# Kernel optimization log

Hardware: AMD Instinct MI355X
Metric: run time of the kernel (lower is better)

## Reference

```python
import jax, jax.numpy as jnp
import numpy as np


def setup_inputs() -> dict:
    key = jax.random.key(0)
    ks = jax.random.split(key, 6)
    B, C, H, W = 8, 128, 64, 64
    return {
        "curr_features": jax.random.normal(ks[0], (B, C, H, W), jnp.float32),
        "w1": jax.random.normal(ks[1], (C, 2 * C), jnp.float32) * 0.05,   # conv1x1 (2C->C)
        "b1": jnp.zeros((C,), jnp.float32),
        "gamma": jnp.ones((C,), jnp.float32),
        "beta": jnp.zeros((C,), jnp.float32),
        "running_mean": jax.random.normal(ks[2], (C,), jnp.float32) * 0.1,
        "running_var": jax.random.uniform(ks[3], (C,), jnp.float32, 0.5, 1.5),
        "w2": jax.random.normal(ks[4], (1, C), jnp.float32) * 0.05,       # conv1x1 (C->1)
        "b2": jnp.zeros((1,), jnp.float32),
    }


def reference(curr_features, w1, b1, gamma, beta, running_mean, running_var, w2, b2):
    B, C, H, W = curr_features.shape
    M = H * W
    BN_EPS = 1e-5
    LEAKY_SLOPE = 0.01  # InPlaceABNSync default activation: leaky_relu(0.01)

    f = curr_features.reshape(B, C, M)                       # [B,C,M]
    scores = jnp.einsum('bcm,bcn->bmn', f, f) * (C ** -0.5)  # [B,M,M]
    p = jax.nn.softmax(scores, axis=-1)
    feats1 = jnp.einsum('bmn,bcn->bcm', p, f)                # [B,C,M]

    x = jnp.concatenate([feats1, f], axis=1).reshape(B, 2 * C, H, W)

    # cls head: conv1x1 -> BN(inference) -> leaky_relu -> (dropout=identity in eval) -> conv1x1
    y = jnp.einsum('oc,bchw->bohw', w1, x) + b1[None, :, None, None]
    scale = gamma / jnp.sqrt(running_var + BN_EPS)
    y = (y - running_mean[None, :, None, None]) * scale[None, :, None, None] + beta[None, :, None, None]
    y = jnp.where(y >= 0, y, LEAKY_SLOPE * y)
    pred = jnp.einsum('oc,bchw->bohw', w2, y) + b2[None, :, None, None]  # [B,1,H,W]
    return pred
```

## Files before the change

kernel.cpp:

```cpp
#include <hip/hip_runtime.h>

#define NB 8
#define NC 128
#define NM 4096
#define FRAG 512

typedef __attribute__((ext_vector_type(8))) short short8;
typedef __attribute__((ext_vector_type(4))) float floatx4;

#define MFMA(a, b, c) __builtin_amdgcn_mfma_f32_16x16x32_bf16(a, b, c, 0, 0, 0)
#define EXP2F(x) __builtin_amdgcn_exp2f(x)

union S8U { short8 v; uint2 u2[2]; };

__device__ __forceinline__ unsigned pack2bf(float a, float b) {
    unsigned ua = __float_as_uint(a);
    unsigned ub = __float_as_uint(b);
    ua += 0x7fffu + ((ua >> 16) & 1u);
    ub += 0x7fffu + ((ub >> 16) & 1u);
    return (ua >> 16) | (ub & 0xffff0000u);
}

__device__ __forceinline__ unsigned cvt_pk_bf16(float a, float b) {
    unsigned r;
    asm("v_cvt_pk_bf16_f32 %0, %1, %2" : "=v"(r) : "v"(a), "v"(b));
    return r;
}

__constant__ float SF_C = 0.35712442f;
__constant__ float RS_C = 2.8001530f;


__global__ __launch_bounds__(256) void k_prep_f(
    const float* __restrict__ f, unsigned short* __restrict__ fX)
{
    __shared__ float Ls[128][65];
    const int tid = threadIdx.x;
    const int b   = blockIdx.x & 7;
    const int m0  = (blockIdx.x >> 3) * 64;
    const float* fb = f + (size_t)b * NC * NM;
    #pragma unroll
    for (int k = 0; k < 32; ++k) {
        int idx = tid + k * 256;
        int c = idx >> 6, mm = idx & 63;
        Ls[c][mm] = fb[(size_t)c * NM + m0 + mm];
    }
    __syncthreads();
    const float sf = SF_C;
    const int m  = tid >> 2;
    const int ks = tid & 3;
    const int ch = ks * 32;
    unsigned pk[16];
    #pragma unroll
    for (int i = 0; i < 16; ++i)
        pk[i] = pack2bf(Ls[ch + 2 * i][m] * sf, Ls[ch + 2 * i + 1][m] * sf);
    const int Mg  = m0 + m;
    const int mt  = Mg >> 4;
    const int lmm = Mg & 15;
    unsigned short* dst = fX + ((size_t)b * 256 + mt) * 4 * FRAG + ks * FRAG;
    #pragma unroll
    for (int q = 0; q < 4; ++q)
        *(uint4*)(dst + (q * 16 + lmm) * 8) =
            make_uint4(pk[4 * q], pk[4 * q + 1], pk[4 * q + 2], pk[4 * q + 3]);
}

__global__ __launch_bounds__(256) void k_prep_g(
    const unsigned short* __restrict__ fX, const float* __restrict__ w1,
    unsigned short* __restrict__ gX)
{
    __shared__ unsigned short gt[128][136];
    const int tid = threadIdx.x;
    const int wv  = tid >> 6;
    const int l   = tid & 63;
    const int lm  = l & 15;
    const int lq  = l >> 4;
    const int b    = blockIdx.x & 7;
    const int nblk = blockIdx.x >> 3;

    const float rs = RS_C;

    short8 wf2[2][4];
    #pragma unroll
    for (int j = 0; j < 2; ++j) {
        const int o = (wv * 2 + j) * 16 + lm;
        #pragma unroll
        for (int ks = 0; ks < 4; ++ks) {
            const float* wp = w1 + (size_t)o * (2 * NC) + ks * 32 + lq * 8;
            S8U t;
            t.u2[0] = make_uint2(pack2bf(wp[0] * rs, wp[1] * rs),
                                 pack2bf(wp[2] * rs, wp[3] * rs));
            t.u2[1] = make_uint2(pack2bf(wp[4] * rs, wp[5] * rs),
                                 pack2bf(wp[6] * rs, wp[7] * rs));
            wf2[j][ks] = t.v;
        }
    }

    const unsigned short* fXb = fX + (size_t)b * NM * NC;
    #pragma unroll 2
    for (int nt = 0; nt < 8; ++nt) {
        short8 af[4];
        #pragma unroll
        for (int ks = 0; ks < 4; ++ks)
            af[ks] = *(const short8*)
                (fXb + (size_t)(nblk * 8 + nt) * 4 * FRAG + ks * FRAG + l * 8);
        #pragma unroll
        for (int j = 0; j < 2; ++j) {
            floatx4 D = {0.f, 0.f, 0.f, 0.f};
            #pragma unroll
            for (int ks = 0; ks < 4; ++ks)
                D = MFMA(af[ks], wf2[j][ks], D);
            *(uint2*)&gt[(wv * 2 + j) * 16 + lm][nt * 16 + lq * 4] =
                make_uint2(pack2bf(D[0], D[1]), pack2bf(D[2], D[3]));
        }
    }
    __syncthreads();

    #pragma unroll
    for (int j = 0; j < 2; ++j) {
        const int ot = wv * 2 + j;
        #pragma unroll
        for (int k2 = 0; k2 < 4; ++k2) {
            uint4 v = *(const uint4*)&gt[ot * 16 + lm][k2 * 32 + lq * 8];
            *(uint4*)(gX + (((size_t)b * 32 + nblk) * 8 + ot) * 4 * FRAG
                      + k2 * FRAG + l * 8) = v;
        }
    }
}

__global__ __launch_bounds__(256, 2) void k_attn(
    const unsigned short* __restrict__ fX,
    const unsigned short* __restrict__ gX,
    const float* __restrict__ w1,
    const float* __restrict__ b1v, const float* __restrict__ gammav,
    const float* __restrict__ betav, const float* __restrict__ rmeanv,
    const float* __restrict__ rvarv, const float* __restrict__ w2v,
    const float* __restrict__ b2v, float* __restrict__ out)
{
    __shared__ __align__(16) char Ps[2][16384];
    __shared__ float lpart[4][64];
    __shared__ float opart[4][64];

    const int tid = threadIdx.x;
    const int w   = tid >> 6;
    const int l   = tid & 63;
    const int lm  = l & 15;
    const int lq  = l >> 4;
    const int b   = blockIdx.x & 7;
    const int m0  = (blockIdx.x >> 3) * 64;

    const int lq0 = lq & 1;
    const int lq1 = lq >> 1;
    const int lm3 = lm >> 3;
    const unsigned Xsw = (unsigned)(((lq1 << 1) | lm3) << 4);
    const unsigned wofsA =
        ((((unsigned)(w >> 1) * 4 * 16) + ((unsigned)(2 * (w & 1) + lq1) * 16)
          + (unsigned)lm) * 16 + (unsigned)(8 * lq0)) ^ Xsw;
    const unsigned rofs = ((unsigned)l * 16) ^ ((((unsigned)l >> 3) & 3u) << 4);

    const unsigned short* fXb = fX + (size_t)b * NM * NC;
    const unsigned short* gXb = gX + (size_t)b * NC * NM;

    short8 qf[4][4];
    {
        const int qt0 = m0 >> 4;
        #pragma unroll
        for (int mt = 0; mt < 4; ++mt)
            #pragma unroll
            for (int ks = 0; ks < 4; ++ks)
                qf[mt][ks] = *(const short8*)
                    (fXb + (size_t)(qt0 + mt) * 4 * FRAG + ks * FRAG + l * 8);
    }

    const unsigned short* kpA = fXb + (size_t)w * 4 * FRAG + l * 8;
    const unsigned short* kpB = fXb + (size_t)(4 + w) * 4 * FRAG + l * 8;
    const unsigned short* gp0 = gXb + (size_t)(2 * w) * 4 * FRAG + l * 8;
    const unsigned short* gp1 = gXb + (size_t)(2 * w + 1) * 4 * FRAG + l * 8;

    short8 kfA[4], kfB[4], gf0[4], gf1[4];
    #pragma unroll
    for (int ks = 0; ks < 4; ++ks) {
        kfA[ks] = *(const short8*)(kpA + ks * FRAG);
        kfB[ks] = *(const short8*)(kpB + ks * FRAG);
    }
    #pragma unroll
    for (int k2 = 0; k2 < 4; ++k2) {
        gf0[k2] = *(const short8*)(gp0 + k2 * FRAG);
        gf1[k2] = *(const short8*)(gp1 + k2 * FRAG);
    }

    floatx4 u[4][2];
    float lsum[4] = {0.f, 0.f, 0.f, 0.f};
    #pragma unroll
    for (int mt = 0; mt < 4; ++mt) {
        u[mt][0] = (floatx4){0.f, 0.f, 0.f, 0.f};
        u[mt][1] = (floatx4){0.f, 0.f, 0.f, 0.f};
    }

    floatx4 svA[4], svB[4];
    #pragma unroll
    for (int mt = 0; mt < 4; ++mt) {
        floatx4 a = {-24.f, -24.f, -24.f, -24.f};
        floatx4 bb = {-24.f, -24.f, -24.f, -24.f};
        #pragma unroll
        for (int ks = 0; ks < 4; ++ks) {
            a  = MFMA(kfA[ks], qf[mt][ks], a);
            bb = MFMA(kfB[ks], qf[mt][ks], bb);
        }
        svA[mt] = a; svB[mt] = bb;
    }
    kpA += 8 * 4 * FRAG; kpB += 8 * 4 * FRAG;
    #pragma unroll
    for (int ks = 0; ks < 4; ++ks) {
        kfA[ks] = *(const short8*)(kpA + ks * FRAG);
        kfB[ks] = *(const short8*)(kpB + ks * FRAG);
    }

    for (int it = 0; it < 32; ++it) {
        const int buf = it & 1;
        char* psb = Ps[buf];

        #pragma unroll
        for (int mt = 0; mt < 4; ++mt) {
            float pA0 = EXP2F(svA[mt][0]);
            float pA1 = EXP2F(svA[mt][1]);
            float pA2 = EXP2F(svA[mt][2]);
            float pA3 = EXP2F(svA[mt][3]);
            float pB0 = EXP2F(svB[mt][0]);
            float pB1 = EXP2F(svB[mt][1]);
            float pB2 = EXP2F(svB[mt][2]);
            float pB3 = EXP2F(svB[mt][3]);
            lsum[mt] += ((pA0 + pA1) + (pA2 + pA3)) +
                        ((pB0 + pB1) + (pB2 + pB3));
            *(uint2*)(psb + mt * 4096 + wofsA) =
                make_uint2(cvt_pk_bf16(pA0, pA1), cvt_pk_bf16(pA2, pA3));
            *(uint2*)(psb + mt * 4096 + wofsA + 2048) =
                make_uint2(cvt_pk_bf16(pB0, pB1), cvt_pk_bf16(pB2, pB3));

            floatx4 a = {-24.f, -24.f, -24.f, -24.f};
            floatx4 bb = {-24.f, -24.f, -24.f, -24.f};
            __builtin_amdgcn_s_setprio(1);
            #pragma unroll
            for (int ks = 0; ks < 4; ++ks) {
                a  = MFMA(kfA[ks], qf[mt][ks], a);
                bb = MFMA(kfB[ks], qf[mt][ks], bb);
            }
            __builtin_amdgcn_s_setprio(0);
            svA[mt] = a; svB[mt] = bb;
        }
        __syncthreads();

        {
            const int kstep = (it < 30) ? 8 * 4 * FRAG : 0;
            kpA += kstep; kpB += kstep;
            #pragma unroll
            for (int ks = 0; ks < 4; ++ks) {
                kfA[ks] = *(const short8*)(kpA + ks * FRAG);
                kfB[ks] = *(const short8*)(kpB + ks * FRAG);
            }
        }

        #pragma unroll
        for (int k2 = 0; k2 < 4; ++k2) {
            short8 pf[4];
            #pragma unroll
            for (int mt = 0; mt < 4; ++mt)
                pf[mt] = *(const short8*)(psb + mt * 4096 + k2 * 1024 + rofs);
            __builtin_amdgcn_s_setprio(1);
            #pragma unroll
            for (int mt = 0; mt < 4; ++mt) {
                u[mt][0] = MFMA(pf[mt], gf0[k2], u[mt][0]);
                u[mt][1] = MFMA(pf[mt], gf1[k2], u[mt][1]);
            }
            __builtin_amdgcn_s_setprio(0);
        }
        {
            const int gstep = (it < 31) ? 8 * 4 * FRAG : 0;
            gp0 += gstep; gp1 += gstep;
            #pragma unroll
            for (int k2 = 0; k2 < 4; ++k2) {
                gf0[k2] = *(const short8*)(gp0 + k2 * FRAG);
                gf1[k2] = *(const short8*)(gp1 + k2 * FRAG);
            }
        }
    }

    #pragma unroll
    for (int mt = 0; mt < 4; ++mt) {
        lsum[mt] += __shfl_xor(lsum[mt], 16);
        lsum[mt] += __shfl_xor(lsum[mt], 32);
    }
    if (lq == 0) {
        #pragma unroll
        for (int mt = 0; mt < 4; ++mt)
            lpart[w][mt * 16 + lm] = lsum[mt];
    }

    floatx4 hacc[4][2];
    {
        const float rs = RS_C;
        #pragma unroll
        for (int j = 0; j < 2; ++j) {
            int o = w * 32 + j * 16 + lm;
            short8 wf[4];
            #pragma unroll
            for (int ks = 0; ks < 4; ++ks) {
                const float* wp = w1 + (size_t)o * (2 * NC) + NC + ks * 32 + lq * 8;
                S8U t;
                t.u2[0] = make_uint2(pack2bf(wp[0] * rs, wp[1] * rs),
                                     pack2bf(wp[2] * rs, wp[3] * rs));
                t.u2[1] = make_uint2(pack2bf(wp[4] * rs, wp[5] * rs),
                                     pack2bf(wp[6] * rs, wp[7] * rs));
                wf[ks] = t.v;
            }
            #pragma unroll
            for (int mt = 0; mt < 4; ++mt) {
                floatx4 a = {0.f, 0.f, 0.f, 0.f};
                #pragma unroll
                for (int ks = 0; ks < 4; ++ks)
                    a = MFMA(qf[mt][ks], wf[ks], a);
                hacc[mt][j] = a;
            }
        }
    }
    __syncthreads();

    float Abn[2], Dbn[2], W2[2];
    #pragma unroll
    for (int j = 0; j < 2; ++j) {
        int o = w * 32 + j * 16 + lm;
        float Ar = gammav[o] * rsqrtf(rvarv[o] + 1e-5f);
        Abn[j] = Ar;
        Dbn[j] = (b1v[o] - rmeanv[o]) * Ar + betav[o];
        W2[j]  = w2v[o];
    }
    float av[16];
    #pragma unroll
    for (int mt = 0; mt < 4; ++mt) {
        float4 L0 = *(const float4*)&lpart[0][mt * 16 + lq * 4];
        float4 L1 = *(const float4*)&lpart[1][mt * 16 + lq * 4];
        float4 L2 = *(const float4*)&lpart[2][mt * 16 + lq * 4];
        float4 L3 = *(const float4*)&lpart[3][mt * 16 + lq * 4];
        float4 Lt;
        Lt.x = (L0.x + L1.x) + (L2.x + L3.x);
        Lt.y = (L0.y + L1.y) + (L2.y + L3.y);
        Lt.z = (L0.z + L1.z) + (L2.z + L3.z);
        Lt.w = (L0.w + L1.w) + (L2.w + L3.w);
        #pragma unroll
        for (int r = 0; r < 4; ++r) {
            float rl = 1.f / ((const float*)&Lt)[r];
            float t0 = Abn[0] * (u[mt][0][r] * rl + hacc[mt][0][r]) + Dbn[0];
            float t1 = Abn[1] * (u[mt][1][r] * rl + hacc[mt][1][r]) + Dbn[1];
            t0 = t0 >= 0.f ? t0 : 0.01f * t0;
            t1 = t1 >= 0.f ? t1 : 0.01f * t1;
            av[mt * 4 + r] = W2[0] * t0 + W2[1] * t1;
        }
    }
    #pragma unroll
    for (int i = 0; i < 16; ++i) {
        av[i] += __shfl_xor(av[i], 1);
        av[i] += __shfl_xor(av[i], 2);
        av[i] += __shfl_xor(av[i], 4);
        av[i] += __shfl_xor(av[i], 8);
    }
    if (lm == 0) {
        #pragma unroll
        for (int mt = 0; mt < 4; ++mt)
            #pragma unroll
            for (int r = 0; r < 4; ++r)
                opart[w][mt * 16 + lq * 4 + r] = av[mt * 4 + r];
    }
    __syncthreads();
    if (tid < 64)
        out[(size_t)b * NM + m0 + tid] =
            b2v[0] + opart[0][tid] + opart[1][tid] + opart[2][tid] + opart[3][tid];
}

extern "C" void kernel_launch(void* const* d_in, const int* in_sizes, int n_in,
                              void* d_out, int out_size, void* d_ws, size_t ws_size,
                              hipStream_t stream) {
    const float* f     = (const float*)d_in[0];
    const float* w1    = (const float*)d_in[1];
    const float* b1    = (const float*)d_in[2];
    const float* gamma = (const float*)d_in[3];
    const float* beta  = (const float*)d_in[4];
    const float* rmean = (const float*)d_in[5];
    const float* rvar  = (const float*)d_in[6];
    const float* w2    = (const float*)d_in[7];
    const float* b2    = (const float*)d_in[8];
    float* out = (float*)d_out;

    unsigned short* fX = (unsigned short*)d_ws;
    unsigned short* gX = fX + (size_t)NB * NM * NC;

    hipLaunchKernelGGL(k_prep_f, dim3(512), dim3(256), 0, stream, f, fX);
    hipLaunchKernelGGL(k_prep_g, dim3(256), dim3(256), 0, stream, fX, w1, gX);
    hipLaunchKernelGGL(k_attn,   dim3(512), dim3(256), 0, stream,
                       fX, gX, w1, b1, gamma, beta, rmean, rvar, w2, b2, out);
}
```

Baseline: 157.7 us.

## Software-pipeline attention loop with double-buffered V fragments and skewed P stages

```diff
diff --git a/kernel.cpp b/kernel.cpp
--- a/kernel.cpp
+++ b/kernel.cpp
@@ -176,7 +176,8 @@
     const unsigned short* gp0 = gXb + (size_t)(2 * w) * 4 * FRAG + l * 8;
     const unsigned short* gp1 = gXb + (size_t)(2 * w + 1) * 4 * FRAG + l * 8;
 
-    short8 kfA[4], kfB[4], gf0[4], gf1[4];
+    short8 kfA[4], kfB[4];
+    short8 gA0[4], gA1[4], gB0[4], gB1[4];
     #pragma unroll
     for (int ks = 0; ks < 4; ++ks) {
         kfA[ks] = *(const short8*)(kpA + ks * FRAG);
@@ -184,8 +185,8 @@
     }
     #pragma unroll
     for (int k2 = 0; k2 < 4; ++k2) {
-        gf0[k2] = *(const short8*)(gp0 + k2 * FRAG);
-        gf1[k2] = *(const short8*)(gp1 + k2 * FRAG);
+        gA0[k2] = *(const short8*)(gp0 + k2 * FRAG);
+        gA1[k2] = *(const short8*)(gp1 + k2 * FRAG);
     }
 
     floatx4 u[4][2];
@@ -196,29 +197,28 @@
         u[mt][1] = (floatx4){0.f, 0.f, 0.f, 0.f};
     }
 
-    floatx4 svA[4], svB[4];
-    #pragma unroll
-    for (int mt = 0; mt < 4; ++mt) {
-        floatx4 a = {-24.f, -24.f, -24.f, -24.f};
-        floatx4 bb = {-24.f, -24.f, -24.f, -24.f};
+    {
+        floatx4 svA[4], svB[4];
+        __builtin_amdgcn_s_setprio(1);
+        #pragma unroll
+        for (int mt = 0; mt < 4; ++mt) {
+            floatx4 a = {-24.f, -24.f, -24.f, -24.f};
+            floatx4 bb = {-24.f, -24.f, -24.f, -24.f};
+            #pragma unroll
+            for (int ks = 0; ks < 4; ++ks) {
+                a  = MFMA(kfA[ks], qf[mt][ks], a);
+                bb = MFMA(kfB[ks], qf[mt][ks], bb);
+            }
+            svA[mt] = a; svB[mt] = bb;
+        }
+        __builtin_amdgcn_s_setprio(0);
+        kpA += 8 * 4 * FRAG; kpB += 8 * 4 * FRAG;
         #pragma unroll
         for (int ks = 0; ks < 4; ++ks) {
-            a  = MFMA(kfA[ks], qf[mt][ks], a);
-            bb = MFMA(kfB[ks], qf[mt][ks], bb);
-        }
-        svA[mt] = a; svB[mt] = bb;
-    }
-    kpA += 8 * 4 * FRAG; kpB += 8 * 4 * FRAG;
-    #pragma unroll
-    for (int ks = 0; ks < 4; ++ks) {
-        kfA[ks] = *(const short8*)(kpA + ks * FRAG);
-        kfB[ks] = *(const short8*)(kpB + ks * FRAG);
-    }
-
-    for (int it = 0; it < 32; ++it) {
-        const int buf = it & 1;
-        char* psb = Ps[buf];
-
+            kfA[ks] = *(const short8*)(kpA + ks * FRAG);
+            kfB[ks] = *(const short8*)(kpB + ks * FRAG);
+        }
+        char* psb = Ps[0];
         #pragma unroll
         for (int mt = 0; mt < 4; ++mt) {
             float pA0 = EXP2F(svA[mt][0]);
@@ -235,53 +235,94 @@
                 make_uint2(cvt_pk_bf16(pA0, pA1), cvt_pk_bf16(pA2, pA3));
             *(uint2*)(psb + mt * 4096 + wofsA + 2048) =
                 make_uint2(cvt_pk_bf16(pB0, pB1), cvt_pk_bf16(pB2, pB3));
-
+        }
+        __syncthreads();
+    }
+
+    auto body = [&](char* psW, char* psR,
+                    short8 (&gC0)[4], short8 (&gC1)[4],
+                    short8 (&gN0)[4], short8 (&gN1)[4], bool loadK) {
+        floatx4 svA[4], svB[4];
+        __builtin_amdgcn_s_setprio(1);
+        #pragma unroll
+        for (int mt = 0; mt < 4; ++mt) {
             floatx4 a = {-24.f, -24.f, -24.f, -24.f};
             floatx4 bb = {-24.f, -24.f, -24.f, -24.f};
-            __builtin_amdgcn_s_setprio(1);
             #pragma unroll
             for (int ks = 0; ks < 4; ++ks) {
                 a  = MFMA(kfA[ks], qf[mt][ks], a);
                 bb = MFMA(kfB[ks], qf[mt][ks], bb);
             }
-            __builtin_amdgcn_s_setprio(0);
             svA[mt] = a; svB[mt] = bb;
         }
-        __syncthreads();
-
-        {
-            const int kstep = (it < 30) ? 8 * 4 * FRAG : 0;
-            kpA += kstep; kpB += kstep;
+        __builtin_amdgcn_s_setprio(0);
+        if (loadK) {
+            kpA += 8 * 4 * FRAG; kpB += 8 * 4 * FRAG;
             #pragma unroll
             for (int ks = 0; ks < 4; ++ks) {
                 kfA[ks] = *(const short8*)(kpA + ks * FRAG);
                 kfB[ks] = *(const short8*)(kpB + ks * FRAG);
             }
         }
-
+        gp0 += 8 * 4 * FRAG; gp1 += 8 * 4 * FRAG;
+        #pragma unroll
+        for (int k2 = 0; k2 < 4; ++k2) {
+            gN0[k2] = *(const short8*)(gp0 + k2 * FRAG);
+            gN1[k2] = *(const short8*)(gp1 + k2 * FRAG);
+        }
+        #pragma unroll
+        for (int mt = 0; mt < 4; ++mt) {
+            float pA0 = EXP2F(svA[mt][0]);
+            float pA1 = EXP2F(svA[mt][1]);
+            float pA2 = EXP2F(svA[mt][2]);
+            float pA3 = EXP2F(svA[mt][3]);
+            float pB0 = EXP2F(svB[mt][0]);
+            float pB1 = EXP2F(svB[mt][1]);
+            float pB2 = EXP2F(svB[mt][2]);
+            float pB3 = EXP2F(svB[mt][3]);
+            lsum[mt] += ((pA0 + pA1) + (pA2 + pA3)) +
+                        ((pB0 + pB1) + (pB2 + pB3));
+            *(uint2*)(psW + mt * 4096 + wofsA) =
+                make_uint2(cvt_pk_bf16(pA0, pA1), cvt_pk_bf16(pA2, pA3));
+            *(uint2*)(psW + mt * 4096 + wofsA + 2048) =
+                make_uint2(cvt_pk_bf16(pB0, pB1), cvt_pk_bf16(pB2, pB3));
+        }
         #pragma unroll
         for (int k2 = 0; k2 < 4; ++k2) {
             short8 pf[4];
             #pragma unroll
             for (int mt = 0; mt < 4; ++mt)
-                pf[mt] = *(const short8*)(psb + mt * 4096 + k2 * 1024 + rofs);
+                pf[mt] = *(const short8*)(psR + mt * 4096 + k2 * 1024 + rofs);
             __builtin_amdgcn_s_setprio(1);
             #pragma unroll
             for (int mt = 0; mt < 4; ++mt) {
-                u[mt][0] = MFMA(pf[mt], gf0[k2], u[mt][0]);
-                u[mt][1] = MFMA(pf[mt], gf1[k2], u[mt][1]);
+                u[mt][0] = MFMA(pf[mt], gC0[k2], u[mt][0]);
+                u[mt][1] = MFMA(pf[mt], gC1[k2], u[mt][1]);
             }
             __builtin_amdgcn_s_setprio(0);
         }
-        {
-            const int gstep = (it < 31) ? 8 * 4 * FRAG : 0;
-            gp0 += gstep; gp1 += gstep;
-            #pragma unroll
-            for (int k2 = 0; k2 < 4; ++k2) {
-                gf0[k2] = *(const short8*)(gp0 + k2 * FRAG);
-                gf1[k2] = *(const short8*)(gp1 + k2 * FRAG);
-            }
-        }
+        __syncthreads();
+    };
+
+    for (int i = 0; i < 15; ++i) {
+        body(Ps[1], Ps[0], gA0, gA1, gB0, gB1, true);
+        body(Ps[0], Ps[1], gB0, gB1, gA0, gA1, true);
+    }
+    body(Ps[1], Ps[0], gA0, gA1, gB0, gB1, false);
+
+    #pragma unroll
+    for (int k2 = 0; k2 < 4; ++k2) {
+        short8 pf[4];
+        #pragma unroll
+        for (int mt = 0; mt < 4; ++mt)
+            pf[mt] = *(const short8*)(Ps[1] + mt * 4096 + k2 * 1024 + rofs);
+        __builtin_amdgcn_s_setprio(1);
+        #pragma unroll
+        for (int mt = 0; mt < 4; ++mt) {
+            u[mt][0] = MFMA(pf[mt], gB0[k2], u[mt][0]);
+            u[mt][1] = MFMA(pf[mt], gB1[k2], u[mt][1]);
+        }
+        __builtin_amdgcn_s_setprio(0);
     }
 
     #pragma unroll
```

Measured after the change: 153.9 us. 2.4% less time.
